# Optimization experiments

Hardware: AMD Instinct MI355X
Metric: run time of the kernel (lower is better)

## Reference

```python
import jax, jax.numpy as jnp
import numpy as np

ALPHA = 0.7
BETTA = 0.3
EPS = 1e-8


def _unit(v):
    n = jnp.linalg.norm(v, axis=-1, keepdims=True)
    return v / jnp.where(n > 0, n, 1.0)


def setup_inputs() -> dict:
    key = jax.random.key(0)
    k1, k2 = jax.random.split(key)
    N, D = 2097152, 3
    vec_1 = jax.random.normal(k1, (N, D), dtype=jnp.float32)
    vec_2 = jax.random.normal(k2, (N, D), dtype=jnp.float32)
    return {"vec_1": vec_1, "vec_2": vec_2}


def reference(vec_1, vec_2):
    # Row mask: keep rows where ||vec_1|| > 1e-8. Instead of boolean gather
    # (data-dependent shape), weight rows by the mask and divide by the count.
    norm1 = jnp.linalg.norm(vec_1, axis=-1, keepdims=True)  # [N,1]
    mask = (norm1 > EPS).astype(vec_1.dtype)                # [N,1]

    n1 = _unit(vec_1)                                       # [N,3]
    u2 = _unit(vec_2)
    # angle between vec_1 and vec_2 (RotationVectors.angle)
    cos_sim = jnp.clip(jnp.sum(n1 * u2, axis=-1), -1.0, 1.0)  # [N]
    a = jnp.arccos(cos_sim)
    # orthonormal companion: Gram-Schmidt of vec_2 against n1
    n2 = _unit(vec_2 - n1 * jnp.sum(n1 * vec_2, axis=-1, keepdims=True))

    sin_a = jnp.sin(a)[:, None]            # [N,1]
    cos_a_m1 = (jnp.cos(a) - 1.0)[:, None]  # [N,1]

    # bmm(M, ones) is just the row-sum of M. For M = x yT the row-sum is
    # x * sum(y), so we never materialize the [N,3,3] outer products:
    s1 = jnp.sum(n1, axis=-1, keepdims=True)  # [N,1]
    s2 = jnp.sum(n2, axis=-1, keepdims=True)
    u_ta = sin_a * (n2 * s1 - n1 * s2)        # transform_a @ ones, [N,3]
    u_tb = cos_a_m1 * (n1 * s1 + n2 * s2)     # transform_b @ ones, [N,3]
    # I @ ones == ones, so mse(I@ones, ones) == 0 elementwise.
    per_row = ALPHA * u_ta ** 2 + BETTA * u_tb ** 2  # [N,3]

    cnt = jnp.maximum(jnp.sum(mask), 1.0)
    loss = jnp.sum(per_row * mask, axis=0) / cnt     # mean over kept rows -> [3]
    return jnp.nan_to_num(loss, nan=0.0, posinf=0.1, neginf=-0.1)
```

## Files before the change

kernel.cpp:

```cpp
#include <hip/hip_runtime.h>
#include <math.h>

#define ALPHA 0.7f
#define BETTA 0.3f
#define EPS   1e-8f

typedef float vfloat4 __attribute__((ext_vector_type(4)));

__device__ __forceinline__ void row_contrib(float x1, float y1, float z1,
                                            float x2, float y2, float z2,
                                            float& a0, float& a1, float& a2,
                                            float& ac) {
    float q1 = x1 * x1 + y1 * y1 + z1 * z1;
    float m = (q1 > EPS * EPS) ? 1.0f : 0.0f;
    float inv1 = (q1 > 0.0f) ? rsqrtf(q1) : 0.0f;
    float n1x = x1 * inv1, n1y = y1 * inv1, n1z = z1 * inv1;

    float q2 = x2 * x2 + y2 * y2 + z2 * z2;
    float inv2 = (q2 > 0.0f) ? rsqrtf(q2) : 0.0f;
    float u2x = x2 * inv2, u2y = y2 * inv2, u2z = z2 * inv2;

    float c = n1x * u2x + n1y * u2y + n1z * u2z;
    c = fminf(1.0f, fmaxf(-1.0f, c));
    float sin_a = sqrtf(fmaxf(0.0f, 1.0f - c * c));
    float cm1 = c - 1.0f;

    float d = n1x * x2 + n1y * y2 + n1z * z2;
    float wx = x2 - n1x * d, wy = y2 - n1y * d, wz = z2 - n1z * d;
    float wq = wx * wx + wy * wy + wz * wz;
    float invw = (wq > 0.0f) ? rsqrtf(wq) : 0.0f;
    float n2x = wx * invw, n2y = wy * invw, n2z = wz * invw;

    float s1 = n1x + n1y + n1z;
    float s2 = n2x + n2y + n2z;

    float tax = sin_a * (n2x * s1 - n1x * s2);
    float tay = sin_a * (n2y * s1 - n1y * s2);
    float taz = sin_a * (n2z * s1 - n1z * s2);

    float tbx = cm1 * (n1x * s1 + n2x * s2);
    float tby = cm1 * (n1y * s1 + n2y * s2);
    float tbz = cm1 * (n1z * s1 + n2z * s2);

    a0 += (ALPHA * tax * tax + BETTA * tbx * tbx) * m;
    a1 += (ALPHA * tay * tay + BETTA * tby * tby) * m;
    a2 += (ALPHA * taz * taz + BETTA * tbz * tbz) * m;
    ac += m;
}

__global__ __launch_bounds__(256) void trl_reduce(const float* __restrict__ v1,
                                                  const float* __restrict__ v2,
                                                  float4* __restrict__ ws,
                                                  int n_rows) {
    int tid = blockIdx.x * blockDim.x + threadIdx.x;
    long row0 = (long)tid * 8;

    float a0 = 0.0f, a1 = 0.0f, a2 = 0.0f, ac = 0.0f;

    if (row0 + 7 < n_rows) {
        const vfloat4* p1 = (const vfloat4*)(v1 + row0 * 3);
        const vfloat4* p2 = (const vfloat4*)(v2 + row0 * 3);
        vfloat4 A[6], B[6];
#pragma unroll
        for (int i = 0; i < 6; ++i) A[i] = __builtin_nontemporal_load(p1 + i);
#pragma unroll
        for (int i = 0; i < 6; ++i) B[i] = __builtin_nontemporal_load(p2 + i);

        row_contrib(A[0].x, A[0].y, A[0].z, B[0].x, B[0].y, B[0].z, a0, a1, a2, ac);
        row_contrib(A[0].w, A[1].x, A[1].y, B[0].w, B[1].x, B[1].y, a0, a1, a2, ac);
        row_contrib(A[1].z, A[1].w, A[2].x, B[1].z, B[1].w, B[2].x, a0, a1, a2, ac);
        row_contrib(A[2].y, A[2].z, A[2].w, B[2].y, B[2].z, B[2].w, a0, a1, a2, ac);
        row_contrib(A[3].x, A[3].y, A[3].z, B[3].x, B[3].y, B[3].z, a0, a1, a2, ac);
        row_contrib(A[3].w, A[4].x, A[4].y, B[3].w, B[4].x, B[4].y, a0, a1, a2, ac);
        row_contrib(A[4].z, A[4].w, A[5].x, B[4].z, B[4].w, B[5].x, a0, a1, a2, ac);
        row_contrib(A[5].y, A[5].z, A[5].w, B[5].y, B[5].z, B[5].w, a0, a1, a2, ac);
    } else {
        for (long r = row0; r < n_rows && r < row0 + 8; ++r) {
            const float* q1 = v1 + r * 3;
            const float* q2 = v2 + r * 3;
            row_contrib(q1[0], q1[1], q1[2], q2[0], q2[1], q2[2], a0, a1, a2, ac);
        }
    }

    for (int off = 32; off > 0; off >>= 1) {
        a0 += __shfl_down(a0, off, 64);
        a1 += __shfl_down(a1, off, 64);
        a2 += __shfl_down(a2, off, 64);
        ac += __shfl_down(ac, off, 64);
    }

    __shared__ float smem[4][4];
    int lane = threadIdx.x & 63;
    int wave = threadIdx.x >> 6;
    if (lane == 0) {
        smem[wave][0] = a0;
        smem[wave][1] = a1;
        smem[wave][2] = a2;
        smem[wave][3] = ac;
    }
    __syncthreads();
    if (threadIdx.x == 0) {
        float4 t;
        t.x = smem[0][0] + smem[1][0] + smem[2][0] + smem[3][0];
        t.y = smem[0][1] + smem[1][1] + smem[2][1] + smem[3][1];
        t.z = smem[0][2] + smem[1][2] + smem[2][2] + smem[3][2];
        t.w = smem[0][3] + smem[1][3] + smem[2][3] + smem[3][3];
        ws[blockIdx.x] = t;
    }
}

__global__ __launch_bounds__(256) void trl_final(const float4* __restrict__ ws,
                                                 float* __restrict__ out,
                                                 int nblocks) {
    float s0 = 0.0f, s1 = 0.0f, s2 = 0.0f, sc = 0.0f;
    for (int i = threadIdx.x; i < nblocks; i += 256) {
        float4 t = ws[i];
        s0 += t.x; s1 += t.y; s2 += t.z; sc += t.w;
    }
    for (int off = 32; off > 0; off >>= 1) {
        s0 += __shfl_down(s0, off, 64);
        s1 += __shfl_down(s1, off, 64);
        s2 += __shfl_down(s2, off, 64);
        sc += __shfl_down(sc, off, 64);
    }
    __shared__ float smem[4][4];
    int lane = threadIdx.x & 63;
    int wave = threadIdx.x >> 6;
    if (lane == 0) {
        smem[wave][0] = s0;
        smem[wave][1] = s1;
        smem[wave][2] = s2;
        smem[wave][3] = sc;
    }
    __syncthreads();
    if (threadIdx.x < 3) {
        float num = smem[0][threadIdx.x] + smem[1][threadIdx.x] +
                    smem[2][threadIdx.x] + smem[3][threadIdx.x];
        float cnt = smem[0][3] + smem[1][3] + smem[2][3] + smem[3][3];
        cnt = fmaxf(cnt, 1.0f);
        float v = num / cnt;
        if (isnan(v)) v = 0.0f;
        else if (isinf(v)) v = (v > 0.0f) ? 0.1f : -0.1f;
        out[threadIdx.x] = v;
    }
}

extern "C" void kernel_launch(void* const* d_in, const int* in_sizes, int n_in,
                              void* d_out, int out_size, void* d_ws, size_t ws_size,
                              hipStream_t stream) {
    const float* v1 = (const float*)d_in[0];
    const float* v2 = (const float*)d_in[1];
    float* out = (float*)d_out;
    float4* ws = (float4*)d_ws;

    int n_rows = in_sizes[0] / 3;

    int block = 256;
    int groups = (n_rows + 7) / 8;
    int grid = (groups + block - 1) / block;

    trl_reduce<<<grid, block, 0, stream>>>(v1, v2, ws, n_rows);
    trl_final<<<1, 256, 0, stream>>>(ws, out, grid);
}
```

Baseline: 101.7 us.

## Stage coalesced float4 tile loads through LDS and halve rows per thread

Each block now loads a contiguous tile with fully coalesced float4 reads (consecutive threads read consecutive float4s), stores it to shared memory, then each thread reads back its own 3 float4s to process 4 rows. Before, each thread read 6 strided float4s per input directly from global memory, with nontemporal hints. This is meant to improve global memory coalescing, at the cost of an LDS round trip, a barrier, and twice as many blocks (and partial sums) since rows per thread drop from 8 to 4. The nontemporal load hint is dropped.

```diff
diff --git a/kernel.cpp b/kernel.cpp
--- a/kernel.cpp
+++ b/kernel.cpp
@@ -5,7 +5,10 @@
 #define BETTA 0.3f
 #define EPS   1e-8f
 
-typedef float vfloat4 __attribute__((ext_vector_type(4)));
+#define BLOCK 256
+#define ROWS_PER_THREAD 4
+#define TILE_ROWS (BLOCK * ROWS_PER_THREAD)
+#define TILE_F4   (TILE_ROWS * 3 / 4)
 
 __device__ __forceinline__ void row_contrib(float x1, float y1, float z1,
                                             float x2, float y2, float z2,
@@ -48,34 +51,52 @@
     ac += m;
 }
 
-__global__ __launch_bounds__(256) void trl_reduce(const float* __restrict__ v1,
-                                                  const float* __restrict__ v2,
-                                                  float4* __restrict__ ws,
-                                                  int n_rows) {
-    int tid = blockIdx.x * blockDim.x + threadIdx.x;
-    long row0 = (long)tid * 8;
+__global__ __launch_bounds__(BLOCK) void trl_reduce(const float* __restrict__ v1,
+                                                    const float* __restrict__ v2,
+                                                    float4* __restrict__ ws,
+                                                    int n_rows) {
+    __shared__ float4 ldsA[TILE_F4];
+    __shared__ float4 ldsB[TILE_F4];
+
+    int t = threadIdx.x;
+    long tile_row0 = (long)blockIdx.x * TILE_ROWS;
 
     float a0 = 0.0f, a1 = 0.0f, a2 = 0.0f, ac = 0.0f;
 
-    if (row0 + 7 < n_rows) {
-        const vfloat4* p1 = (const vfloat4*)(v1 + row0 * 3);
-        const vfloat4* p2 = (const vfloat4*)(v2 + row0 * 3);
-        vfloat4 A[6], B[6];
-#pragma unroll
-        for (int i = 0; i < 6; ++i) A[i] = __builtin_nontemporal_load(p1 + i);
-#pragma unroll
-        for (int i = 0; i < 6; ++i) B[i] = __builtin_nontemporal_load(p2 + i);
+    if (tile_row0 + TILE_ROWS <= n_rows) {
+        const float4* g1 = (const float4*)v1;
+        const float4* g2 = (const float4*)v2;
+        long base = (long)blockIdx.x * TILE_F4;
 
-        row_contrib(A[0].x, A[0].y, A[0].z, B[0].x, B[0].y, B[0].z, a0, a1, a2, ac);
-        row_contrib(A[0].w, A[1].x, A[1].y, B[0].w, B[1].x, B[1].y, a0, a1, a2, ac);
-        row_contrib(A[1].z, A[1].w, A[2].x, B[1].z, B[1].w, B[2].x, a0, a1, a2, ac);
-        row_contrib(A[2].y, A[2].z, A[2].w, B[2].y, B[2].z, B[2].w, a0, a1, a2, ac);
-        row_contrib(A[3].x, A[3].y, A[3].z, B[3].x, B[3].y, B[3].z, a0, a1, a2, ac);
-        row_contrib(A[3].w, A[4].x, A[4].y, B[3].w, B[4].x, B[4].y, a0, a1, a2, ac);
-        row_contrib(A[4].z, A[4].w, A[5].x, B[4].z, B[4].w, B[5].x, a0, a1, a2, ac);
-        row_contrib(A[5].y, A[5].z, A[5].w, B[5].y, B[5].z, B[5].w, a0, a1, a2, ac);
+        float4 la0 = g1[base + 0 * BLOCK + t];
+        float4 la1 = g1[base + 1 * BLOCK + t];
+        float4 la2 = g1[base + 2 * BLOCK + t];
+        float4 lb0 = g2[base + 0 * BLOCK + t];
+        float4 lb1 = g2[base + 1 * BLOCK + t];
+        float4 lb2 = g2[base + 2 * BLOCK + t];
+
+        ldsA[0 * BLOCK + t] = la0;
+        ldsA[1 * BLOCK + t] = la1;
+        ldsA[2 * BLOCK + t] = la2;
+        ldsB[0 * BLOCK + t] = lb0;
+        ldsB[1 * BLOCK + t] = lb1;
+        ldsB[2 * BLOCK + t] = lb2;
+        __syncthreads();
+
+        float4 A0 = ldsA[3 * t + 0];
+        float4 A1 = ldsA[3 * t + 1];
+        float4 A2 = ldsA[3 * t + 2];
+        float4 B0 = ldsB[3 * t + 0];
+        float4 B1 = ldsB[3 * t + 1];
+        float4 B2 = ldsB[3 * t + 2];
+
+        row_contrib(A0.x, A0.y, A0.z, B0.x, B0.y, B0.z, a0, a1, a2, ac);
+        row_contrib(A0.w, A1.x, A1.y, B0.w, B1.x, B1.y, a0, a1, a2, ac);
+        row_contrib(A1.z, A1.w, A2.x, B1.z, B1.w, B2.x, a0, a1, a2, ac);
+        row_contrib(A2.y, A2.z, A2.w, B2.y, B2.z, B2.w, a0, a1, a2, ac);
     } else {
-        for (long r = row0; r < n_rows && r < row0 + 8; ++r) {
+        long row0 = tile_row0 + (long)t * ROWS_PER_THREAD;
+        for (long r = row0; r < n_rows && r < row0 + ROWS_PER_THREAD; ++r) {
             const float* q1 = v1 + r * 3;
             const float* q2 = v2 + r * 3;
             row_contrib(q1[0], q1[1], q1[2], q2[0], q2[1], q2[2], a0, a1, a2, ac);
@@ -90,8 +111,8 @@
     }
 
     __shared__ float smem[4][4];
-    int lane = threadIdx.x & 63;
-    int wave = threadIdx.x >> 6;
+    int lane = t & 63;
+    int wave = t >> 6;
     if (lane == 0) {
         smem[wave][0] = a0;
         smem[wave][1] = a1;
@@ -99,13 +120,13 @@
         smem[wave][3] = ac;
     }
     __syncthreads();
-    if (threadIdx.x == 0) {
-        float4 t;
-        t.x = smem[0][0] + smem[1][0] + smem[2][0] + smem[3][0];
-        t.y = smem[0][1] + smem[1][1] + smem[2][1] + smem[3][1];
-        t.z = smem[0][2] + smem[1][2] + smem[2][2] + smem[3][2];
-        t.w = smem[0][3] + smem[1][3] + smem[2][3] + smem[3][3];
-        ws[blockIdx.x] = t;
+    if (t == 0) {
+        float4 o;
+        o.x = smem[0][0] + smem[1][0] + smem[2][0] + smem[3][0];
+        o.y = smem[0][1] + smem[1][1] + smem[2][1] + smem[3][1];
+        o.z = smem[0][2] + smem[1][2] + smem[2][2] + smem[3][2];
+        o.w = smem[0][3] + smem[1][3] + smem[2][3] + smem[3][3];
+        ws[blockIdx.x] = o;
     }
 }
 
@@ -114,8 +135,8 @@
                                                  int nblocks) {
     float s0 = 0.0f, s1 = 0.0f, s2 = 0.0f, sc = 0.0f;
     for (int i = threadIdx.x; i < nblocks; i += 256) {
-        float4 t = ws[i];
-        s0 += t.x; s1 += t.y; s2 += t.z; sc += t.w;
+        float4 p = ws[i];
+        s0 += p.x; s1 += p.y; s2 += p.z; sc += p.w;
     }
     for (int off = 32; off > 0; off >>= 1) {
         s0 += __shfl_down(s0, off, 64);
@@ -155,10 +176,8 @@
 
     int n_rows = in_sizes[0] / 3;
 
-    int block = 256;
-    int groups = (n_rows + 7) / 8;
-    int grid = (groups + block - 1) / block;
+    int grid = (n_rows + TILE_ROWS - 1) / TILE_ROWS;
 
-    trl_reduce<<<grid, block, 0, stream>>>(v1, v2, ws, n_rows);
+    trl_reduce<<<grid, BLOCK, 0, stream>>>(v1, v2, ws, n_rows);
     trl_final<<<1, 256, 0, stream>>>(ws, out, grid);
 }
```

Measured after the change: 89.87 us. 1.13x faster.
